# Optimization experiments

Hardware: AMD Instinct MI355X
Metric: run time of the kernel (lower is better)

Reference implementation:

```python
import jax, jax.numpy as jnp
import numpy as np
from jax import lax

HIDDEN = 128

def setup_inputs() -> dict:
    key = jax.random.key(0)
    ks = jax.random.split(key, 8)
    B, S, V, D = 256, 512, 50000, 300
    x = jax.random.randint(ks[0], (B, S), 0, V, dtype=jnp.int64)
    emb = jax.random.normal(ks[1], (V, D), dtype=jnp.float32)
    s_ih = 1.0 / np.sqrt(HIDDEN)
    W_ih = jax.random.normal(ks[2], (HIDDEN, D), dtype=jnp.float32) * s_ih
    W_hh = jax.random.normal(ks[3], (HIDDEN, HIDDEN), dtype=jnp.float32) * s_ih
    b_ih = jax.random.normal(ks[4], (HIDDEN,), dtype=jnp.float32) * s_ih
    b_hh = jax.random.normal(ks[5], (HIDDEN,), dtype=jnp.float32) * s_ih
    fc_w = jax.random.normal(ks[6], (1, 2 * HIDDEN), dtype=jnp.float32) * (1.0 / np.sqrt(2 * HIDDEN))
    fc_b = jax.random.normal(ks[7], (1,), dtype=jnp.float32) * 0.01
    return {"x": x, "emb": emb, "W_ih": W_ih, "W_hh": W_hh,
            "b_ih": b_ih, "b_hh": b_hh, "fc_w": fc_w, "fc_b": fc_b}

def reference(x, emb, W_ih, W_hh, b_ih, b_hh, fc_w, fc_b):
    # Embedding lookup: [B,S] -> [B,S,D]
    xe = emb[x]
    # Precompute input projection for all timesteps: [B,S,H]
    xp = jnp.einsum('bsd,hd->bsh', xe, W_ih) + b_ih
    B = xp.shape[0]
    h0 = jnp.zeros((B, HIDDEN), dtype=xp.dtype)

    def step(h, xt):  # xt: [B,H]
        h = jnp.tanh(xt + h @ W_hh.T + b_hh)
        return h, h

    _, outs = lax.scan(step, h0, xp.transpose(1, 0, 2))  # outs: [S,B,H]
    outs = outs.transpose(1, 0, 2)  # [B,S,H]
    pooled = jnp.concatenate([outs.max(axis=1), outs.mean(axis=1)], axis=-1)  # [B,2H]
    return pooled @ fc_w.T + fc_b  # [B,1]
```

## Files before the change

kernel.cpp:

```cpp
#include <hip/hip_runtime.h>

#define HID    128
#define SEQ    512
#define BATCH  256
#define DIM    300
#define VOCAB  50000

typedef short bf16x8 __attribute__((ext_vector_type(8)));
typedef float f32x4  __attribute__((ext_vector_type(4)));

#define KP   320
#define LST  328

__device__ __forceinline__ unsigned bf16_rtne(float v)
{
    unsigned u = __float_as_uint(v);
    return (u + 0x7FFFu + ((u >> 16) & 1u)) >> 16;
}

__global__ __launch_bounds__(512)
void proj_mfma(const float* __restrict__ emb,
               const float* __restrict__ Wih,
               const float* __restrict__ bih,
               const float* __restrict__ bhh,
               float* __restrict__ P)
{
    __shared__ unsigned short At[64 * LST];
    __shared__ unsigned short Bt[128 * LST];

    const int t  = threadIdx.x;
    const int v0 = blockIdx.x * 64;

    for (int c = t; c < 64 * 40; c += 512) {
        const int row = c / 40;
        const int ch  = c - row * 40;
        int grow = v0 + row; if (grow > VOCAB - 1) grow = VOCAB - 1;
        const float* src = emb + (size_t)grow * DIM;
        const int k0 = ch * 8;
        unsigned p0, p1, p2, p3;
        if (k0 + 8 <= DIM) {
            const float4 a = *(const float4*)(src + k0);
            const float4 b = *(const float4*)(src + k0 + 4);
            p0 = bf16_rtne(a.x) | (bf16_rtne(a.y) << 16);
            p1 = bf16_rtne(a.z) | (bf16_rtne(a.w) << 16);
            p2 = bf16_rtne(b.x) | (bf16_rtne(b.y) << 16);
            p3 = bf16_rtne(b.z) | (bf16_rtne(b.w) << 16);
        } else {
            unsigned q[8];
            #pragma unroll
            for (int e = 0; e < 8; ++e) {
                const int k = k0 + e;
                q[e] = (k < DIM) ? bf16_rtne(src[k]) : 0u;
            }
            p0 = q[0] | (q[1] << 16);  p1 = q[2] | (q[3] << 16);
            p2 = q[4] | (q[5] << 16);  p3 = q[6] | (q[7] << 16);
        }
        uint4 o = {p0, p1, p2, p3};
        *(uint4*)(&At[row * LST + k0]) = o;
    }

    for (int c = t; c < 128 * 40; c += 512) {
        const int row = c / 40;
        const int ch  = c - row * 40;
        const float* src = Wih + (size_t)row * DIM;
        const int k0 = ch * 8;
        unsigned p0, p1, p2, p3;
        if (k0 + 8 <= DIM) {
            const float4 a = *(const float4*)(src + k0);
            const float4 b = *(const float4*)(src + k0 + 4);
            p0 = bf16_rtne(a.x) | (bf16_rtne(a.y) << 16);
            p1 = bf16_rtne(a.z) | (bf16_rtne(a.w) << 16);
            p2 = bf16_rtne(b.x) | (bf16_rtne(b.y) << 16);
            p3 = bf16_rtne(b.z) | (bf16_rtne(b.w) << 16);
        } else {
            unsigned q[8];
            #pragma unroll
            for (int e = 0; e < 8; ++e) {
                const int k = k0 + e;
                q[e] = (k < DIM) ? bf16_rtne(src[k]) : 0u;
            }
            p0 = q[0] | (q[1] << 16);  p1 = q[2] | (q[3] << 16);
            p2 = q[4] | (q[5] << 16);  p3 = q[6] | (q[7] << 16);
        }
        uint4 o = {p0, p1, p2, p3};
        *(uint4*)(&Bt[row * LST + k0]) = o;
    }
    __syncthreads();

    const int lane = t & 63;
    const int w    = t >> 6;
    const int mt   = w >> 1;
    const int nh   = w & 1;
    const int lm   = lane & 15;
    const int kg   = lane >> 4;

    f32x4 acc0 = {0.f,0.f,0.f,0.f}, acc1 = {0.f,0.f,0.f,0.f};
    f32x4 acc2 = {0.f,0.f,0.f,0.f}, acc3 = {0.f,0.f,0.f,0.f};

    const unsigned short* arow = &At[(mt * 16 + lm) * LST + kg * 8];
    const unsigned short* brow = &Bt[(nh * 64 + lm) * LST + kg * 8];

    for (int k0 = 0; k0 < KP; k0 += 32) {
        const bf16x8 af = *(const bf16x8*)(arow + k0);
        const bf16x8 b0 = *(const bf16x8*)(brow + k0);
        const bf16x8 b1 = *(const bf16x8*)(brow + 16 * LST + k0);
        const bf16x8 b2 = *(const bf16x8*)(brow + 32 * LST + k0);
        const bf16x8 b3 = *(const bf16x8*)(brow + 48 * LST + k0);
        acc0 = __builtin_amdgcn_mfma_f32_16x16x32_bf16(af, b0, acc0, 0, 0, 0);
        acc1 = __builtin_amdgcn_mfma_f32_16x16x32_bf16(af, b1, acc1, 0, 0, 0);
        acc2 = __builtin_amdgcn_mfma_f32_16x16x32_bf16(af, b2, acc2, 0, 0, 0);
        acc3 = __builtin_amdgcn_mfma_f32_16x16x32_bf16(af, b3, acc3, 0, 0, 0);
    }

    const int rbase = v0 + mt * 16 + kg * 4;
    #pragma unroll
    for (int nt = 0; nt < 4; ++nt) {
        const int h = nh * 64 + nt * 16 + lm;
        const float bb = bih[h] + bhh[h];
        const f32x4 a = (nt == 0) ? acc0 : (nt == 1) ? acc1 : (nt == 2) ? acc2 : acc3;
        #pragma unroll
        for (int r = 0; r < 4; ++r) {
            const int row = rbase + r;
            if (row < VOCAB) P[(size_t)row * HID + h] = a[r] + bb;
        }
    }
}

__device__ __forceinline__ float quad_sum(float v)
{
    int x1 = __builtin_amdgcn_update_dpp(0, __float_as_int(v), 0xB1, 0xF, 0xF, true);
    v += __int_as_float(x1);
    int x2 = __builtin_amdgcn_update_dpp(0, __float_as_int(v), 0x4E, 0xF, 0xF, true);
    v += __int_as_float(x2);
    return v;
}

__global__ __launch_bounds__(512)
void rnn_kernel(const int* __restrict__ x,
                const float* __restrict__ Whh,
                const float* __restrict__ P,
                const float* __restrict__ fcw,
                const float* __restrict__ fcb,
                float* __restrict__ out)
{
    __shared__ float h0b[HID];
    __shared__ float h1b[HID];
    __shared__ int   toff[SEQ];
    __shared__ float xb[2 * 64 * HID];
    __shared__ float red[HID];

    const int t  = threadIdx.x;
    const int b  = blockIdx.x;
    const int i  = t >> 2;
    const int kq = t & 3;

    toff[t] = x[b * SEQ + t] * HID;
    if (t < HID) h0b[t] = 0.f;

    float4 w[8];
    #pragma unroll
    for (int j = 0; j < 8; ++j) {
        const int pj = (j + 2 * kq) & 7;
        w[j] = *(const float4*)(Whh + (size_t)i * HID + kq * 32 + pj * 4);
    }
    __syncthreads();

#define STAGE(cn) do {                                                        \
        const int w_ = t >> 6, l_ = t & 63;                                   \
        const int base_ = ((cn) & 1) * (64 * HID);                            \
        _Pragma("unroll")                                                     \
        for (int q_ = 0; q_ < 4; ++q_) {                                      \
            const int row_ = w_ * 8 + q_ * 2 + (l_ >> 5);                     \
            const int col_ = (l_ & 31) * 4;                                   \
            const int off_ = toff[(cn) * 64 + row_] + col_;                   \
            const float4 v_ = *(const float4*)(P + off_);                     \
            *(float4*)(&xb[base_ + row_ * HID + col_]) = v_;                  \
        }                                                                     \
    } while (0)

    STAGE(0);
    __syncthreads();

    float hmax = -3.0e38f, hsum = 0.f;

#define STEP(HRD, HWR, XPTR, SOFF) do {                                       \
        const float xt = (XPTR)[(SOFF) * HID];                                \
        float ac0=0.f,ac1=0.f,ac2=0.f,ac3=0.f,ac4=0.f,ac5=0.f,ac6=0.f,ac7=0.f;\
        _Pragma("unroll")                                                     \
        for (int j = 0; j < 8; ++j) {                                         \
            const int pj = (j + 2 * kq) & 7;                                  \
            const float4 h4 = *(const float4*)((HRD) + kq * 32 + pj * 4);     \
            float* ap = (j==0)?&ac0:(j==1)?&ac1:(j==2)?&ac2:(j==3)?&ac3       \
                       :(j==4)?&ac4:(j==5)?&ac5:(j==6)?&ac6:&ac7;             \
            *ap = fmaf(w[j].x, h4.x, *ap);                                    \
            *ap = fmaf(w[j].y, h4.y, *ap);                                    \
            *ap = fmaf(w[j].z, h4.z, *ap);                                    \
            *ap = fmaf(w[j].w, h4.w, *ap);                                    \
        }                                                                     \
        float acc = ((ac0+ac1)+(ac2+ac3)) + ((ac4+ac5)+(ac6+ac7));            \
        acc = quad_sum(acc);                                                  \
        const float z = xt + acc;                                             \
        const float e = __builtin_amdgcn_exp2f(z * 2.8853900817779268f);      \
        const float hnew = fmaf(-2.f, __builtin_amdgcn_rcpf(e + 1.f), 1.f);   \
        hmax = fmaxf(hmax, hnew);                                             \
        hsum += hnew;                                                         \
        (HWR)[i] = hnew;                                                      \
        __syncthreads();                                                      \
    } while (0)

    for (int c = 0; c < 8; ++c) {
        if (c < 7) STAGE(c + 1);
        const float* xp = &xb[(c & 1) * (64 * HID) + i];
        #pragma unroll 4
        for (int u = 0; u < 32; ++u) {
            STEP(h0b, h1b, xp, u * 2);
            STEP(h1b, h0b, xp, u * 2 + 1);
        }
    }
#undef STEP
#undef STAGE

    if (kq == 0)
        red[i] = fcw[i] * hmax + fcw[HID + i] * (hsum * (1.f / 512.f));
    __syncthreads();
    if (t < 64) {
        float v = red[t] + red[t + 64];
        #pragma unroll
        for (int m = 32; m >= 1; m >>= 1) v += __shfl_xor(v, m);
        if (t == 0) out[b] = v + fcb[0];
    }
}

extern "C" void kernel_launch(void* const* d_in, const int* in_sizes, int n_in,
                              void* d_out, int out_size, void* d_ws, size_t ws_size,
                              hipStream_t stream)
{
    const int*   x   = (const int*)  d_in[0];
    const float* emb = (const float*)d_in[1];
    const float* Wih = (const float*)d_in[2];
    const float* Whh = (const float*)d_in[3];
    const float* bih = (const float*)d_in[4];
    const float* bhh = (const float*)d_in[5];
    const float* fcw = (const float*)d_in[6];
    const float* fcb = (const float*)d_in[7];

    float* P = (float*)d_ws;

    proj_mfma<<<(VOCAB + 63) / 64, 512, 0, stream>>>(emb, Wih, bih, bhh, P);
    rnn_kernel<<<BATCH, 512, 0, stream>>>(x, Whh, P, fcw, fcb, (float*)d_out);
}
```

Baseline: 228.1 us.

## Make vocab projection persistent with double-buffered embedding staging

Replaces the one-block-per-64-rows projection kernel with a persistent grid of 256 blocks. Each block converts W_ih to bf16 once and loops over 32-row vocab tiles, staging the next tile's embedding rows into a second LDS buffer while MFMAs run on the current one. This is meant to amortise the repeated W_ih load and conversion across tiles and to overlap global loads with compute. In exchange, each wave computes a smaller tile, which may lower MFMA density, and a block barrier runs every tile.

```diff
diff --git a/kernel.cpp b/kernel.cpp
--- a/kernel.cpp
+++ b/kernel.cpp
@@ -9,8 +9,10 @@
 typedef short bf16x8 __attribute__((ext_vector_type(8)));
 typedef float f32x4  __attribute__((ext_vector_type(4)));
 
-#define KP   320
-#define LST  328
+#define KP     320
+#define LST    328
+#define TROWS  32
+#define NTILES ((VOCAB + TROWS - 1) / TROWS)
 
 __device__ __forceinline__ unsigned bf16_rtne(float v)
 {
@@ -19,45 +21,17 @@
 }
 
 __global__ __launch_bounds__(512)
-void proj_mfma(const float* __restrict__ emb,
-               const float* __restrict__ Wih,
-               const float* __restrict__ bih,
-               const float* __restrict__ bhh,
-               float* __restrict__ P)
-{
-    __shared__ unsigned short At[64 * LST];
+void proj_persist(const float* __restrict__ emb,
+                  const float* __restrict__ Wih,
+                  const float* __restrict__ bih,
+                  const float* __restrict__ bhh,
+                  float* __restrict__ P)
+{
     __shared__ unsigned short Bt[128 * LST];
-
-    const int t  = threadIdx.x;
-    const int v0 = blockIdx.x * 64;
-
-    for (int c = t; c < 64 * 40; c += 512) {
-        const int row = c / 40;
-        const int ch  = c - row * 40;
-        int grow = v0 + row; if (grow > VOCAB - 1) grow = VOCAB - 1;
-        const float* src = emb + (size_t)grow * DIM;
-        const int k0 = ch * 8;
-        unsigned p0, p1, p2, p3;
-        if (k0 + 8 <= DIM) {
-            const float4 a = *(const float4*)(src + k0);
-            const float4 b = *(const float4*)(src + k0 + 4);
-            p0 = bf16_rtne(a.x) | (bf16_rtne(a.y) << 16);
-            p1 = bf16_rtne(a.z) | (bf16_rtne(a.w) << 16);
-            p2 = bf16_rtne(b.x) | (bf16_rtne(b.y) << 16);
-            p3 = bf16_rtne(b.z) | (bf16_rtne(b.w) << 16);
-        } else {
-            unsigned q[8];
-            #pragma unroll
-            for (int e = 0; e < 8; ++e) {
-                const int k = k0 + e;
-                q[e] = (k < DIM) ? bf16_rtne(src[k]) : 0u;
-            }
-            p0 = q[0] | (q[1] << 16);  p1 = q[2] | (q[3] << 16);
-            p2 = q[4] | (q[5] << 16);  p3 = q[6] | (q[7] << 16);
-        }
-        uint4 o = {p0, p1, p2, p3};
-        *(uint4*)(&At[row * LST + k0]) = o;
-    }
+    __shared__ unsigned short At[2 * TROWS * LST];
+
+    const int t   = threadIdx.x;
+    const int bid = blockIdx.x;
 
     for (int c = t; c < 128 * 40; c += 512) {
         const int row = c / 40;
@@ -85,45 +59,83 @@
         uint4 o = {p0, p1, p2, p3};
         *(uint4*)(&Bt[row * LST + k0]) = o;
     }
-    __syncthreads();
+
+#define STAGE_EMB(tl, bf) do {                                                \
+        const int v0_ = (tl) * TROWS;                                         \
+        for (int c = t; c < TROWS * 40; c += 512) {                           \
+            const int row = c / 40;                                           \
+            const int ch  = c - row * 40;                                     \
+            int grow = v0_ + row; if (grow > VOCAB - 1) grow = VOCAB - 1;     \
+            const float* src = emb + (size_t)grow * DIM;                      \
+            const int k0 = ch * 8;                                            \
+            unsigned p0, p1, p2, p3;                                          \
+            if (k0 + 8 <= DIM) {                                              \
+                const float4 a = *(const float4*)(src + k0);                  \
+                const float4 b = *(const float4*)(src + k0 + 4);              \
+                p0 = bf16_rtne(a.x) | (bf16_rtne(a.y) << 16);                 \
+                p1 = bf16_rtne(a.z) | (bf16_rtne(a.w) << 16);                 \
+                p2 = bf16_rtne(b.x) | (bf16_rtne(b.y) << 16);                 \
+                p3 = bf16_rtne(b.z) | (bf16_rtne(b.w) << 16);                 \
+            } else {                                                          \
+                unsigned q[8];                                                \
+                _Pragma("unroll")                                             \
+                for (int e = 0; e < 8; ++e) {                                 \
+                    const int k = k0 + e;                                     \
+                    q[e] = (k < DIM) ? bf16_rtne(src[k]) : 0u;                \
+                }                                                             \
+                p0 = q[0] | (q[1] << 16);  p1 = q[2] | (q[3] << 16);          \
+                p2 = q[4] | (q[5] << 16);  p3 = q[6] | (q[7] << 16);          \
+            }                                                                 \
+            uint4 o = {p0, p1, p2, p3};                                       \
+            *(uint4*)(&At[(bf) * (TROWS * LST) + row * LST + k0]) = o;        \
+        }                                                                     \
+    } while (0)
 
     const int lane = t & 63;
     const int w    = t >> 6;
-    const int mt   = w >> 1;
-    const int nh   = w & 1;
+    const int mt   = w >> 2;
+    const int np   = w & 3;
     const int lm   = lane & 15;
     const int kg   = lane >> 4;
 
-    f32x4 acc0 = {0.f,0.f,0.f,0.f}, acc1 = {0.f,0.f,0.f,0.f};
-    f32x4 acc2 = {0.f,0.f,0.f,0.f}, acc3 = {0.f,0.f,0.f,0.f};
-
-    const unsigned short* arow = &At[(mt * 16 + lm) * LST + kg * 8];
-    const unsigned short* brow = &Bt[(nh * 64 + lm) * LST + kg * 8];
-
-    for (int k0 = 0; k0 < KP; k0 += 32) {
-        const bf16x8 af = *(const bf16x8*)(arow + k0);
-        const bf16x8 b0 = *(const bf16x8*)(brow + k0);
-        const bf16x8 b1 = *(const bf16x8*)(brow + 16 * LST + k0);
-        const bf16x8 b2 = *(const bf16x8*)(brow + 32 * LST + k0);
-        const bf16x8 b3 = *(const bf16x8*)(brow + 48 * LST + k0);
-        acc0 = __builtin_amdgcn_mfma_f32_16x16x32_bf16(af, b0, acc0, 0, 0, 0);
-        acc1 = __builtin_amdgcn_mfma_f32_16x16x32_bf16(af, b1, acc1, 0, 0, 0);
-        acc2 = __builtin_amdgcn_mfma_f32_16x16x32_bf16(af, b2, acc2, 0, 0, 0);
-        acc3 = __builtin_amdgcn_mfma_f32_16x16x32_bf16(af, b3, acc3, 0, 0, 0);
-    }
-
-    const int rbase = v0 + mt * 16 + kg * 4;
-    #pragma unroll
-    for (int nt = 0; nt < 4; ++nt) {
-        const int h = nh * 64 + nt * 16 + lm;
-        const float bb = bih[h] + bhh[h];
-        const f32x4 a = (nt == 0) ? acc0 : (nt == 1) ? acc1 : (nt == 2) ? acc2 : acc3;
+    STAGE_EMB(bid, 0);
+    __syncthreads();
+
+    int buf = 0;
+    for (int tile = bid; tile < NTILES; tile += 256) {
+        if (tile + 256 < NTILES) STAGE_EMB(tile + 256, buf ^ 1);
+
+        const unsigned short* arow = &At[buf * (TROWS * LST)
+                                         + (mt * 16 + lm) * LST + kg * 8];
+        const unsigned short* brow = &Bt[(np * 32 + lm) * LST + kg * 8];
+
+        f32x4 acc0 = {0.f,0.f,0.f,0.f}, acc1 = {0.f,0.f,0.f,0.f};
         #pragma unroll
-        for (int r = 0; r < 4; ++r) {
-            const int row = rbase + r;
-            if (row < VOCAB) P[(size_t)row * HID + h] = a[r] + bb;
-        }
-    }
+        for (int k0 = 0; k0 < KP; k0 += 32) {
+            const bf16x8 af = *(const bf16x8*)(arow + k0);
+            const bf16x8 b0 = *(const bf16x8*)(brow + k0);
+            const bf16x8 b1 = *(const bf16x8*)(brow + 16 * LST + k0);
+            acc0 = __builtin_amdgcn_mfma_f32_16x16x32_bf16(af, b0, acc0, 0, 0, 0);
+            acc1 = __builtin_amdgcn_mfma_f32_16x16x32_bf16(af, b1, acc1, 0, 0, 0);
+        }
+
+        const int rbase = tile * TROWS + mt * 16 + kg * 4;
+        #pragma unroll
+        for (int nt2 = 0; nt2 < 2; ++nt2) {
+            const int h = (np * 2 + nt2) * 16 + lm;
+            const float bb = bih[h] + bhh[h];
+            const f32x4 a = nt2 ? acc1 : acc0;
+            #pragma unroll
+            for (int r = 0; r < 4; ++r) {
+                const int row = rbase + r;
+                if (row < VOCAB) P[(size_t)row * HID + h] = a[r] + bb;
+            }
+        }
+
+        __syncthreads();
+        buf ^= 1;
+    }
+#undef STAGE_EMB
 }
 
 __device__ __forceinline__ float quad_sum(float v)
@@ -246,6 +258,6 @@
 
     float* P = (float*)d_ws;
 
-    proj_mfma<<<(VOCAB + 63) / 64, 512, 0, stream>>>(emb, Wih, bih, bhh, P);
+    proj_persist<<<256, 512, 0, stream>>>(emb, Wih, bih, bhh, P);
     rnn_kernel<<<BATCH, 512, 0, stream>>>(x, Whh, P, fcw, fcb, (float*)d_out);
 }
```

New measurement: 197.8 us. -13.2%, faster.
